# Kernel tuning notes

Hardware: AMD Instinct MI355X
Metric: run time of the kernel (lower is better)

Reference implementation:

```python
import jax, jax.numpy as jnp
import numpy as np


def setup_inputs() -> dict:
    key = jax.random.key(0)
    k1, k2, k3, k4, k5 = jax.random.split(key, 5)
    B, K, C = 64, 1024, 16
    x = jax.random.normal(k1, (B, 1, K, K), dtype=jnp.float32)
    # conv_row weight [C,1,K,1] -> [C,K]; conv_column weight [C,1,1,K] -> [C,K]
    scale = 1.0 / np.sqrt(K)
    W_row = jax.random.normal(k2, (C, K), dtype=jnp.float32) * scale
    b_row = jax.random.normal(k3, (C,), dtype=jnp.float32) * scale
    W_col = jax.random.normal(k4, (C, K), dtype=jnp.float32) * scale
    b_col = jax.random.normal(k5, (C,), dtype=jnp.float32) * scale
    return {"x": x, "W_row": W_row, "b_row": b_row, "W_col": W_col, "b_col": b_col}


def reference(x, W_row, b_row, W_col, b_col):
    # x: [B,1,K,K] -> squeeze channel
    xs = x[:, 0]  # [B,K,K]
    K = xs.shape[-1]
    # conv_row (kernel Kx1): r[b,c,j] = sum_i W_row[c,i]*x[b,i,j] + b_row[c]  -> [B,C,K]
    r = jnp.einsum('ci,bij->bcj', W_row, xs) + b_row[None, :, None]
    # conv_column (kernel 1xK): col[b,c,i] = sum_j W_col[c,j]*x[b,i,j] + b_col[c] -> [B,C,K]
    col = jnp.einsum('cj,bij->bci', W_col, xs) + b_col[None, :, None]
    # tiled matmul: out[b,c,i,j] = sum_k r[b,c,k]*col[b,c,k] (constant over i,j);
    # torch.diag extracts that scalar K times -> broadcast to [B,C,K]
    s = jnp.einsum('bck,bck->bc', r, col)  # [B,C]
    return jnp.broadcast_to(s[:, :, None], (s.shape[0], s.shape[1], K))
```

## Files before the change

kernel.cpp:

```cpp
#include <hip/hip_runtime.h>
#include <stdint.h>

typedef float  f32x4 __attribute__((ext_vector_type(4)));
typedef short  s16x8 __attribute__((ext_vector_type(8)));

constexpr int Kdim    = 1024;
constexpr int Cdim    = 16;
constexpr int NCHUNK  = 8;
constexpr int ROWS_CH = 128;
constexpr int TROWS   = 32;
constexpr int NTILE   = ROWS_CH / TROWS;
constexpr int RS      = Kdim + 8;

static __device__ __forceinline__ ushort f2bf(float f) {
  uint32_t u = __builtin_bit_cast(uint32_t, f);
  u += 0x7FFFu + ((u >> 16) & 1u);
  return (ushort)(u >> 16);
}
static __device__ __forceinline__ float bf2f(ushort u) {
  return __builtin_bit_cast(float, (uint32_t)u << 16);
}

static __device__ __forceinline__ void bar_lds() {
  __builtin_amdgcn_sched_barrier(0);
  asm volatile("s_waitcnt lgkmcnt(0)" ::: "memory");
  __builtin_amdgcn_s_barrier();
  __builtin_amdgcn_sched_barrier(0);
}

__global__ __launch_bounds__(256, 2) void k_main(const float* __restrict__ x, const float* __restrict__ Wr,
                                                 const float* __restrict__ Wc, ushort* __restrict__ r_bf,
                                                 float* __restrict__ col_ws) {
  __shared__ ushort x_l[TROWS * RS];
  __shared__ float  colp[2][4 * 64 * 4];

  const int t    = threadIdx.x;
  const int lane = t & 63;
  const int w    = t >> 6;
  const int b    = blockIdx.x >> 3;
  const int ch   = blockIdx.x & 7;
  const int i0   = ch * ROWS_CH;
  const float* xb = x + (size_t)b * Kdim * Kdim;
  const float* xt = xb + 4 * t;

  f32x4 pa0, pa1, pa2, pa3, pb0, pb1, pb2, pb3;
  pa0 = *(const f32x4*)(xt + (size_t)(i0 + 0) * Kdim);
  pa1 = *(const f32x4*)(xt + (size_t)(i0 + 1) * Kdim);
  pa2 = *(const f32x4*)(xt + (size_t)(i0 + 2) * Kdim);
  pa3 = *(const f32x4*)(xt + (size_t)(i0 + 3) * Kdim);

  const int kh = w >> 1;
  const int kg = lane >> 4;
  const float* wcrow = Wc + (size_t)(lane & 15) * Kdim;
  s16x8 wfrag[16];
  #pragma unroll
  for (int s = 0; s < 16; ++s) {
    const float* p = wcrow + (kh * 16 + s) * 32 + kg * 8;
    f32x4 lo = *(const f32x4*)p;
    f32x4 hi = *(const f32x4*)(p + 4);
    s16x8 f;
    f[0] = (short)f2bf(lo.x); f[1] = (short)f2bf(lo.y); f[2] = (short)f2bf(lo.z); f[3] = (short)f2bf(lo.w);
    f[4] = (short)f2bf(hi.x); f[5] = (short)f2bf(hi.y); f[6] = (short)f2bf(hi.z); f[7] = (short)f2bf(hi.w);
    wfrag[s] = f;
  }

  float racc[Cdim][4];
  #pragma unroll
  for (int c = 0; c < Cdim; ++c) { racc[c][0] = racc[c][1] = racc[c][2] = racc[c][3] = 0.f; }

  auto proc_row = [&](int row, int grow, f32x4 v) {
    const float* wrp = Wr + grow;
    #pragma unroll
    for (int c = 0; c < Cdim; ++c) {
      const float wv = wrp[(size_t)c * Kdim];
      racc[c][0] = fmaf(wv, v.x, racc[c][0]);
      racc[c][1] = fmaf(wv, v.y, racc[c][1]);
      racc[c][2] = fmaf(wv, v.z, racc[c][2]);
      racc[c][3] = fmaf(wv, v.w, racc[c][3]);
    }
    ushort4 u4 = make_ushort4(f2bf(v.x), f2bf(v.y), f2bf(v.z), f2bf(v.w));
    *(ushort4*)&x_l[row * RS + 4 * t] = u4;
  };

  auto phase_c = [&](int p, int r0p) {
    if (t < 128) {
      const int it = t >> 6;
      const int l  = t & 63;
      f32x4 va = *(const f32x4*)&colp[p][(it * 64 + l) * 4];
      f32x4 vb = *(const f32x4*)&colp[p][((it + 2) * 64 + l) * 4];
      const int c     = l & 15;
      const int rbase = r0p + it * 16 + ((l >> 4) << 2);
      f32x4 o = va + vb;
      *(f32x4*)(col_ws + ((size_t)(b * Cdim + c)) * Kdim + rbase) = o;
    }
  };

  for (int tl = 0; tl < NTILE; ++tl) {
    const int r0 = i0 + tl * TROWS;

    if (tl) phase_c((tl - 1) & 1, r0 - TROWS);

    for (int g = 0; g < 8; g += 2) {
      const int nr1 = r0 + (g + 1) * 4;
      pb0 = *(const f32x4*)(xt + (size_t)(nr1 + 0) * Kdim);
      pb1 = *(const f32x4*)(xt + (size_t)(nr1 + 1) * Kdim);
      pb2 = *(const f32x4*)(xt + (size_t)(nr1 + 2) * Kdim);
      pb3 = *(const f32x4*)(xt + (size_t)(nr1 + 3) * Kdim);
      proc_row(g * 4 + 0, r0 + g * 4 + 0, pa0);
      proc_row(g * 4 + 1, r0 + g * 4 + 1, pa1);
      proc_row(g * 4 + 2, r0 + g * 4 + 2, pa2);
      proc_row(g * 4 + 3, r0 + g * 4 + 3, pa3);
      const int nr2 = r0 + (g + 2) * 4;
      if (g + 2 < 8 || tl + 1 < NTILE) {
        pa0 = *(const f32x4*)(xt + (size_t)(nr2 + 0) * Kdim);
        pa1 = *(const f32x4*)(xt + (size_t)(nr2 + 1) * Kdim);
        pa2 = *(const f32x4*)(xt + (size_t)(nr2 + 2) * Kdim);
        pa3 = *(const f32x4*)(xt + (size_t)(nr2 + 3) * Kdim);
      }
      proc_row(g * 4 + 4, nr1 + 0, pb0);
      proc_row(g * 4 + 5, nr1 + 1, pb1);
      proc_row(g * 4 + 6, nr1 + 2, pb2);
      proc_row(g * 4 + 7, nr1 + 3, pb3);
    }
    bar_lds();

    {
      const int it   = w & 1;
      const int arow = it * 16 + (lane & 15);
      f32x4 acc = {0.f, 0.f, 0.f, 0.f};
      #pragma unroll
      for (int s = 0; s < 16; ++s) {
        const int ks = kh * 16 + s;
        s16x8 a = *(const s16x8*)&x_l[arow * RS + ks * 32 + kg * 8];
        acc = __builtin_amdgcn_mfma_f32_16x16x32_bf16(a, wfrag[s], acc, 0, 0, 0);
      }
      *(f32x4*)&colp[tl & 1][(w * 64 + lane) * 4] = acc;
    }
    bar_lds();
  }
  phase_c((NTILE - 1) & 1, i0 + (NTILE - 1) * TROWS);

  ushort* rp = r_bf + ((size_t)(b * NCHUNK + ch) * Cdim) * Kdim + 4 * t;
  #pragma unroll
  for (int c = 0; c < Cdim; ++c) {
    ushort4 u4 = make_ushort4(f2bf(racc[c][0]), f2bf(racc[c][1]), f2bf(racc[c][2]), f2bf(racc[c][3]));
    *(ushort4*)(rp + (size_t)c * Kdim) = u4;
  }
}

__global__ __launch_bounds__(256) void k_out(const ushort* __restrict__ r_bf, const float* __restrict__ col_ws,
                                             const float* __restrict__ b_row, const float* __restrict__ b_col,
                                             float* __restrict__ out) {
  const int bid = blockIdx.x;
  const int b = bid >> 4, c = bid & 15;
  const int t = threadIdx.x;
  const float br = b_row[c], bc = b_col[c];

  f32x4 rv = {0.f, 0.f, 0.f, 0.f};
  #pragma unroll
  for (int ch = 0; ch < NCHUNK; ++ch) {
    ushort4 u = *(const ushort4*)(r_bf + ((size_t)(b * NCHUNK + ch) * Cdim + c) * Kdim + 4 * t);
    rv.x += bf2f(u.x); rv.y += bf2f(u.y); rv.z += bf2f(u.z); rv.w += bf2f(u.w);
  }
  f32x4 cv = *(const f32x4*)(col_ws + ((size_t)(b * Cdim + c)) * Kdim + 4 * t);
  float part = 0.f;
  #pragma unroll
  for (int q = 0; q < 4; ++q) part += (rv[q] + br) * (cv[q] + bc);

  #pragma unroll
  for (int off = 1; off < 64; off <<= 1) part += __shfl_xor(part, off);
  __shared__ float wsum[4];
  if ((t & 63) == 0) wsum[t >> 6] = part;
  __syncthreads();
  const float s = wsum[0] + wsum[1] + wsum[2] + wsum[3];

  f32x4 o = {s, s, s, s};
  *(f32x4*)(out + ((size_t)(b * Cdim + c)) * Kdim + 4 * t) = o;
}

extern "C" void kernel_launch(void* const* d_in, const int* in_sizes, int n_in,
                              void* d_out, int out_size, void* d_ws, size_t ws_size,
                              hipStream_t stream) {
  const float* x  = (const float*)d_in[0];
  const float* Wr = (const float*)d_in[1];
  const float* br = (const float*)d_in[2];
  const float* Wc = (const float*)d_in[3];
  const float* bc = (const float*)d_in[4];
  float* out = (float*)d_out;

  char* ws = (char*)d_ws;
  ushort* r_bf   = (ushort*)ws;
  float*  col_ws = (float*)(ws + 16777216);

  k_main<<<512, 256, 0, stream>>>(x, Wr, Wc, r_bf, col_ws);
  k_out<<<1024, 256, 0, stream>>>(r_bf, col_ws, br, bc, out);
}
```

Baseline: 60.34 us.

## Fuse row-partial and output kernels with intra-batch spin barrier and last-block reduction

The two-kernel pipeline becomes a single kernel. Each block waits on a per-batch atomic counter until all 8 chunk blocks have written their column projections. It then takes the dot product of its fp32 row partials against the full column vector, writes per-chunk partial sums, and the last block per batch reduces them and writes the broadcast output. This drops the bf16 round-trip of row partials through global memory and the second launch. In exchange it adds a memset, a spin-wait that assumes all 8 blocks of a batch are co-resident (512 blocks at 2 per CU fits on the device), and a serialized output write by one block per batch.

```diff
diff --git a/kernel.cpp b/kernel.cpp
--- a/kernel.cpp
+++ b/kernel.cpp
@@ -17,9 +17,6 @@
   u += 0x7FFFu + ((u >> 16) & 1u);
   return (ushort)(u >> 16);
 }
-static __device__ __forceinline__ float bf2f(ushort u) {
-  return __builtin_bit_cast(float, (uint32_t)u << 16);
-}
 
 static __device__ __forceinline__ void bar_lds() {
   __builtin_amdgcn_sched_barrier(0);
@@ -28,11 +25,15 @@
   __builtin_amdgcn_sched_barrier(0);
 }
 
-__global__ __launch_bounds__(256, 2) void k_main(const float* __restrict__ x, const float* __restrict__ Wr,
-                                                 const float* __restrict__ Wc, ushort* __restrict__ r_bf,
-                                                 float* __restrict__ col_ws) {
+__global__ __launch_bounds__(256, 2) void k_fused(const float* __restrict__ x, const float* __restrict__ Wr,
+                                                  const float* __restrict__ Wc, const float* __restrict__ b_row,
+                                                  const float* __restrict__ b_col, float* __restrict__ col_ws,
+                                                  float* __restrict__ sparts, int* __restrict__ cntA,
+                                                  int* __restrict__ cntB, float* __restrict__ out) {
   __shared__ ushort x_l[TROWS * RS];
   __shared__ float  colp[2][4 * 64 * 4];
+  __shared__ float  wred[4 * Cdim];
+  __shared__ int    lastFlag;
 
   const int t    = threadIdx.x;
   const int lane = t & 63;
@@ -140,42 +141,59 @@
   }
   phase_c((NTILE - 1) & 1, i0 + (NTILE - 1) * TROWS);
 
-  ushort* rp = r_bf + ((size_t)(b * NCHUNK + ch) * Cdim) * Kdim + 4 * t;
+  __threadfence();
+  __syncthreads();
+  if (t == 0) {
+    __hip_atomic_fetch_add(&cntA[b * 4], 1, __ATOMIC_ACQ_REL, __HIP_MEMORY_SCOPE_AGENT);
+    while (__hip_atomic_load(&cntA[b * 4], __ATOMIC_ACQUIRE, __HIP_MEMORY_SCOPE_AGENT) < NCHUNK)
+      __builtin_amdgcn_s_sleep(1);
+  }
+  __syncthreads();
+  { int v = __hip_atomic_load(&cntA[b * 4], __ATOMIC_ACQUIRE, __HIP_MEMORY_SCOPE_AGENT);
+    asm volatile("" :: "v"(v)); }
+
+  const float* clp = col_ws + (size_t)b * Cdim * Kdim + 4 * t;
   #pragma unroll
   for (int c = 0; c < Cdim; ++c) {
-    ushort4 u4 = make_ushort4(f2bf(racc[c][0]), f2bf(racc[c][1]), f2bf(racc[c][2]), f2bf(racc[c][3]));
-    *(ushort4*)(rp + (size_t)c * Kdim) = u4;
-  }
-}
-
-__global__ __launch_bounds__(256) void k_out(const ushort* __restrict__ r_bf, const float* __restrict__ col_ws,
-                                             const float* __restrict__ b_row, const float* __restrict__ b_col,
-                                             float* __restrict__ out) {
-  const int bid = blockIdx.x;
-  const int b = bid >> 4, c = bid & 15;
-  const int t = threadIdx.x;
-  const float br = b_row[c], bc = b_col[c];
-
-  f32x4 rv = {0.f, 0.f, 0.f, 0.f};
-  #pragma unroll
-  for (int ch = 0; ch < NCHUNK; ++ch) {
-    ushort4 u = *(const ushort4*)(r_bf + ((size_t)(b * NCHUNK + ch) * Cdim + c) * Kdim + 4 * t);
-    rv.x += bf2f(u.x); rv.y += bf2f(u.y); rv.z += bf2f(u.z); rv.w += bf2f(u.w);
-  }
-  f32x4 cv = *(const f32x4*)(col_ws + ((size_t)(b * Cdim + c)) * Kdim + 4 * t);
-  float part = 0.f;
-  #pragma unroll
-  for (int q = 0; q < 4; ++q) part += (rv[q] + br) * (cv[q] + bc);
-
-  #pragma unroll
-  for (int off = 1; off < 64; off <<= 1) part += __shfl_xor(part, off);
-  __shared__ float wsum[4];
-  if ((t & 63) == 0) wsum[t >> 6] = part;
-  __syncthreads();
-  const float s = wsum[0] + wsum[1] + wsum[2] + wsum[3];
-
-  f32x4 o = {s, s, s, s};
-  *(f32x4*)(out + ((size_t)(b * Cdim + c)) * Kdim + 4 * t) = o;
+    f32x4 cv = *(const f32x4*)(clp + (size_t)c * Kdim);
+    const float brq = b_row[c] * (1.f / NCHUNK);
+    const float bcv = b_col[c];
+    float p = (racc[c][0] + brq) * (cv.x + bcv) + (racc[c][1] + brq) * (cv.y + bcv)
+            + (racc[c][2] + brq) * (cv.z + bcv) + (racc[c][3] + brq) * (cv.w + bcv);
+    #pragma unroll
+    for (int off = 32; off; off >>= 1) p += __shfl_xor(p, off);
+    if (lane == 0) wred[w * Cdim + c] = p;
+  }
+  __syncthreads();
+  if (t < Cdim)
+    sparts[((size_t)b * NCHUNK + ch) * Cdim + t] =
+        wred[t] + wred[Cdim + t] + wred[2 * Cdim + t] + wred[3 * Cdim + t];
+
+  __threadfence();
+  __syncthreads();
+  if (t == 0) {
+    int old = __hip_atomic_fetch_add(&cntB[b * 4], 1, __ATOMIC_ACQ_REL, __HIP_MEMORY_SCOPE_AGENT);
+    lastFlag = (old == NCHUNK - 1);
+  }
+  __syncthreads();
+  if (!lastFlag) return;
+
+  { int v = __hip_atomic_load(&cntB[b * 4], __ATOMIC_ACQUIRE, __HIP_MEMORY_SCOPE_AGENT);
+    asm volatile("" :: "v"(v)); }
+  if (t < Cdim) {
+    float s = 0.f;
+    #pragma unroll
+    for (int c2 = 0; c2 < NCHUNK; ++c2) s += sparts[((size_t)b * NCHUNK + c2) * Cdim + t];
+    wred[t] = s;
+  }
+  __syncthreads();
+  float* ob = out + (size_t)b * Cdim * Kdim;
+  #pragma unroll
+  for (int i = t; i < Cdim * Kdim / 4; i += 256) {
+    const float s = wred[i >> 8];
+    f32x4 o = {s, s, s, s};
+    *(f32x4*)(ob + 4 * i) = o;
+  }
 }
 
 extern "C" void kernel_launch(void* const* d_in, const int* in_sizes, int n_in,
@@ -189,9 +207,11 @@
   float* out = (float*)d_out;
 
   char* ws = (char*)d_ws;
-  ushort* r_bf   = (ushort*)ws;
-  float*  col_ws = (float*)(ws + 16777216);
-
-  k_main<<<512, 256, 0, stream>>>(x, Wr, Wc, r_bf, col_ws);
-  k_out<<<1024, 256, 0, stream>>>(r_bf, col_ws, br, bc, out);
-}
+  float* col_ws = (float*)ws;
+  float* sparts = (float*)(ws + 4194304);
+  int*   cntA   = (int*)  (ws + 4194304 + 32768);
+  int*   cntB   = (int*)  (ws + 4194304 + 32768 + 1024);
+
+  hipMemsetAsync((void*)cntA, 0, 2048, stream);
+  k_fused<<<64 * NCHUNK, 256, 0, stream>>>(x, Wr, Wc, br, bc, col_ws, sparts, cntA, cntB, out);
+}
```

New measurement: 231.2 us. 3.83x slower.
